# Optimization experiments

Measured on AMD Instinct MI355X. Metric: run time of the kernel, lower is better.

The kernel has to match this reference:

```python
import jax, jax.numpy as jnp
import numpy as np

NUM_HEADS = 8
DIM_OUT = 768
SCALE = DIM_OUT ** (-0.5)


def setup_inputs() -> dict:
    key = jax.random.key(0)
    k1, k2, k3, k4, k5 = jax.random.split(key, 5)
    B, N1, N2, DIM_T, DIM_V, K = 4, 2048, 2048, 768, 1024, 4
    F_t = jax.random.normal(k1, (B, N1, DIM_T), dtype=jnp.float32)
    F_s = jax.random.normal(k2, (B, N2, DIM_V), dtype=jnp.float32)
    # stacked linear_proj weights, stored input-major: x @ W_lin[layer]
    W_lin = jax.random.normal(k3, (K, DIM_V, DIM_T), dtype=jnp.float32) * 0.02
    # conv1d(kernel=1) == pointwise linear, stored input-major: x @ W_q + b_q
    W_q = jax.random.normal(k4, (DIM_T, DIM_OUT), dtype=jnp.float32) * 0.02
    b_q = jax.random.normal(k5, (DIM_OUT,), dtype=jnp.float32) * 0.02
    layer = 1
    return {"F_t": F_t, "F_s": F_s, "W_lin": W_lin, "W_q": W_q, "b_q": b_q, "layer": layer}


def reference(F_t, F_s, W_lin, W_q, b_q, layer):
    B, N1, _ = F_t.shape
    N2 = F_s.shape[1]
    H = NUM_HEADS
    D = DIM_OUT // H  # head_dim

    # per-layer linear projection + L2 normalization of keys/values
    F_s_p = F_s @ W_lin[layer]                                   # [B,N2,dim_t]
    F_s_p = F_s_p / jnp.linalg.norm(F_s_p, axis=-1, keepdims=True)

    # conv1d kernel-size-1 Q projection == pointwise linear
    q = (F_t @ W_q + b_q).reshape(B, N1, H, D)                   # [B,N1,H,D]
    kv = F_s_p.reshape(B, N2, H, D)                              # [B,N2,H,D]

    attn = jnp.einsum('bnhd,bmhd->bhnm', q, kv) * SCALE          # [B,H,N1,N2]
    attn = jax.nn.softmax(attn, axis=-1)

    F_t_a = jnp.einsum('bhnm,bmhd->bnhd', attn, kv).reshape(B, N1, H * D)
    F_t_a = F_t_a + F_t                                          # residual
    F_t_a = F_t_a / jnp.linalg.norm(F_t_a, axis=-1, keepdims=True)
    return (F_t_a, F_s_p)
```

## Files before the change

### kernel.cpp

```cpp
#include <hip/hip_runtime.h>

using short8 = __attribute__((ext_vector_type(8))) short;
using f32x4  = __attribute__((ext_vector_type(4))) float;

#define DEV __device__ __forceinline__

#define GLBP(p) ((const __attribute__((address_space(1))) unsigned int*)(p))
#define LDSP(p) ((__attribute__((address_space(3))) unsigned int*)(p))

#define EXP2F(x) __builtin_amdgcn_exp2f(x)

DEV unsigned short f2bf(float f) {
    unsigned int u = __float_as_uint(f);
    u += 0x7fffu + ((u >> 16) & 1u);
    return (unsigned short)(u >> 16);
}

DEV unsigned int pack2bf(float a, float b) {
    unsigned int ua = __float_as_uint(a);
    ua += 0x7fffu + ((ua >> 16) & 1u);
    unsigned int ub = __float_as_uint(b);
    ub += 0x7fffu + ((ub >> 16) & 1u);
    return (ua >> 16) | (ub & 0xffff0000u);
}

__global__ __launch_bounds__(256) void wt2_k(const float* __restrict__ Wl,
                                             const float* __restrict__ Wq,
                                             unsigned short* __restrict__ outl,
                                             unsigned short* __restrict__ outq,
                                             const int* __restrict__ layerp) {
    const int z = blockIdx.z;
    int R, C;
    const float* in;
    unsigned short* out;
    if (z == 0) {
        R = 1024; C = 768;
        in = Wl + (size_t)layerp[0] * (1024 * 768);
        out = outl;
    } else {
        if (blockIdx.y >= 24) return;
        R = 768; C = 768;
        in = Wq;
        out = outq;
    }
    __shared__ float t[32][33];
    const int tx = threadIdx.x & 31, ty = threadIdx.x >> 5;
    const int c0 = blockIdx.x * 32, r0 = blockIdx.y * 32;
#pragma unroll
    for (int it = 0; it < 4; ++it)
        t[ty + it * 8][tx] = in[(size_t)(r0 + ty + it * 8) * C + c0 + tx];
    __syncthreads();
#pragma unroll
    for (int it = 0; it < 4; ++it)
        out[(size_t)(c0 + ty + it * 8) * R + r0 + tx] = f2bf(t[tx][ty + it * 8]);
}

__global__ __launch_bounds__(256) void kvt_k(const unsigned short* __restrict__ kv,
                                             unsigned short* __restrict__ kvT) {
    const int n0 = blockIdx.x * 32, d0 = blockIdx.y * 32, bh = blockIdx.z;
    const int b = bh >> 3, h = bh & 7;
    __shared__ unsigned short t[32][33];
    const int tx = threadIdx.x & 31, ty = threadIdx.x >> 5;
#pragma unroll
    for (int it = 0; it < 4; ++it)
        t[ty + it * 8][tx] = kv[(size_t)(b * 2048 + n0 + ty + it * 8) * 768 + h * 96 + d0 + tx];
    __syncthreads();
#pragma unroll
    for (int it = 0; it < 4; ++it)
        kvT[((size_t)bh * 96 + d0 + ty + it * 8) * 2048 + n0 + tx] = t[tx][ty + it * 8];
}

__global__ __launch_bounds__(256) void gemm_dual(const float* __restrict__ A0,
                                                 const unsigned short* __restrict__ B0,
                                                 float* __restrict__ C0,
                                                 const float* __restrict__ A1,
                                                 const unsigned short* __restrict__ B1,
                                                 unsigned short* __restrict__ C1,
                                                 const float* __restrict__ bias,
                                                 float oscale) {
    __shared__ unsigned short smA[4096];
    __shared__ unsigned short smB[3072];
    const int z = blockIdx.z;
    const float* A = z ? A1 : A0;
    const unsigned short* B = z ? B1 : B0;
    const int K = z ? 768 : 1024;
    const int tid = threadIdx.x, lane = tid & 63;
    const int l15 = lane & 15, g = lane >> 4;
    const int w = tid >> 6, wm = w >> 1, wn = w & 1;
    const int m0 = blockIdx.x * 128, n0 = blockIdx.y * 96;
    const int srow = tid >> 2, skg = tid & 3;
    const int brow0 = tid % 96, bkg0 = tid / 96;
    const int c1 = tid + 256;
    const int brow1 = c1 % 96, bkg1 = c1 / 96;
    const unsigned short* pB0 = B + (size_t)(n0 + brow0) * K + bkg0 * 8;
    const unsigned short* pB1 = B + (size_t)(n0 + brow1) * K + bkg1 * 8;
    f32x4 acc[4][3] = {};
    const int nkt = K >> 5;
    for (int kt = 0; kt < nkt; ++kt) {
        const int k0 = kt << 5;
        __syncthreads();
        {
            __builtin_amdgcn_global_load_lds(GLBP(pB0 + k0), LDSP(smB + tid * 8), 16, 0, 0);
            if (tid < 128)
                __builtin_amdgcn_global_load_lds(GLBP(pB1 + k0), LDSP(smB + c1 * 8), 16, 0, 0);
            const float* p0 = A + (size_t)(m0 + srow) * K + k0 + skg * 8;
            const float* p1 = A + (size_t)(m0 + 64 + srow) * K + k0 + skg * 8;
            float4 a0 = *(const float4*)p0, a0b = *(const float4*)(p0 + 4);
            float4 a1 = *(const float4*)p1, a1b = *(const float4*)(p1 + 4);
            short8 va0, va1;
            va0[0] = f2bf(a0.x);  va0[1] = f2bf(a0.y);  va0[2] = f2bf(a0.z);  va0[3] = f2bf(a0.w);
            va0[4] = f2bf(a0b.x); va0[5] = f2bf(a0b.y); va0[6] = f2bf(a0b.z); va0[7] = f2bf(a0b.w);
            va1[0] = f2bf(a1.x);  va1[1] = f2bf(a1.y);  va1[2] = f2bf(a1.z);  va1[3] = f2bf(a1.w);
            va1[4] = f2bf(a1b.x); va1[5] = f2bf(a1b.y); va1[6] = f2bf(a1b.z); va1[7] = f2bf(a1b.w);
            *(short8*)(smA + (skg * 128 + srow) * 8) = va0;
            *(short8*)(smA + (skg * 128 + 64 + srow) * 8) = va1;
        }
        __syncthreads();
        short8 af[4], bf[3];
#pragma unroll
        for (int i = 0; i < 4; ++i)
            af[i] = *(const short8*)(smA + (g * 128 + wm * 64 + i * 16 + l15) * 8);
#pragma unroll
        for (int j = 0; j < 3; ++j)
            bf[j] = *(const short8*)(smB + (g * 96 + wn * 48 + j * 16 + l15) * 8);
#pragma unroll
        for (int i = 0; i < 4; ++i)
#pragma unroll
            for (int j = 0; j < 3; ++j)
                acc[i][j] = __builtin_amdgcn_mfma_f32_16x16x32_bf16(af[i], bf[j], acc[i][j], 0, 0, 0);
    }
#pragma unroll
    for (int j = 0; j < 3; ++j) {
        const int col = n0 + wn * 48 + j * 16 + l15;
        const float bv = z ? bias[col] : 0.0f;
#pragma unroll
        for (int i = 0; i < 4; ++i)
#pragma unroll
            for (int r = 0; r < 4; ++r) {
                const int row = m0 + wm * 64 + i * 16 + g * 4 + r;
                if (z == 0) {
                    C0[(size_t)row * 768 + col] = acc[i][j][r];
                } else {
                    const float v = (acc[i][j][r] + bv) * oscale;
                    C1[(size_t)row * 768 + col] = f2bf(v);
                }
            }
    }
}

__global__ __launch_bounds__(256) void rownorm_k(const float* __restrict__ in,
                                                 float* __restrict__ outf,
                                                 unsigned short* __restrict__ outb) {
    const int lane = threadIdx.x & 63;
    const int row = blockIdx.x * 4 + (threadIdx.x >> 6);
    const float* p = in + (size_t)row * 768;
    float4 v[3];
    float s = 0.f;
#pragma unroll
    for (int i = 0; i < 3; ++i) {
        v[i] = ((const float4*)p)[i * 64 + lane];
        s += v[i].x * v[i].x + v[i].y * v[i].y + v[i].z * v[i].z + v[i].w * v[i].w;
    }
#pragma unroll
    for (int mask = 1; mask < 64; mask <<= 1) s += __shfl_xor(s, mask);
    const float inv = rsqrtf(s);
    float4* of = (float4*)(outf + (size_t)row * 768);
    ushort4* ob = (ushort4*)(outb + (size_t)row * 768);
#pragma unroll
    for (int i = 0; i < 3; ++i) {
        float4 q;
        q.x = v[i].x * inv; q.y = v[i].y * inv; q.z = v[i].z * inv; q.w = v[i].w * inv;
        of[i * 64 + lane] = q;
        ushort4 u;
        u.x = f2bf(q.x); u.y = f2bf(q.y); u.z = f2bf(q.z); u.w = f2bf(q.w);
        ob[i * 64 + lane] = u;
    }
}

__global__ __launch_bounds__(256) void resid_norm_k(const unsigned short* __restrict__ in,
                                                    const float* __restrict__ res,
                                                    float* __restrict__ outf) {
    const int lane = threadIdx.x & 63;
    const int row = blockIdx.x * 4 + (threadIdx.x >> 6);
    const ushort4* pa = (const ushort4*)(in + (size_t)row * 768);
    const float4* pb = (const float4*)(res + (size_t)row * 768);
    float4 v[3];
    float s = 0.f;
#pragma unroll
    for (int i = 0; i < 3; ++i) {
        ushort4 a = pa[i * 64 + lane];
        float4 b = pb[i * 64 + lane];
        float4 c;
        c.x = __uint_as_float((unsigned int)a.x << 16) + b.x;
        c.y = __uint_as_float((unsigned int)a.y << 16) + b.y;
        c.z = __uint_as_float((unsigned int)a.z << 16) + b.z;
        c.w = __uint_as_float((unsigned int)a.w << 16) + b.w;
        v[i] = c;
        s += c.x * c.x + c.y * c.y + c.z * c.z + c.w * c.w;
    }
#pragma unroll
    for (int mask = 1; mask < 64; mask <<= 1) s += __shfl_xor(s, mask);
    const float inv = rsqrtf(s);
    float4* of = (float4*)(outf + (size_t)row * 768);
#pragma unroll
    for (int i = 0; i < 3; ++i) {
        float4 q;
        q.x = v[i].x * inv; q.y = v[i].y * inv; q.z = v[i].z * inv; q.w = v[i].w * inv;
        of[i * 64 + lane] = q;
    }
}

__global__ __launch_bounds__(512) void attn_k(const unsigned short* __restrict__ Q,
                                              const unsigned short* __restrict__ KV,
                                              const unsigned short* __restrict__ KVT,
                                              unsigned short* __restrict__ O) {
    __shared__ unsigned short sK[2][6144];
    __shared__ unsigned short sV[2][6144];
    __shared__ unsigned short plds[8][32][72];
    const int hw = blockIdx.x;
    const int bid = (hw & 7) * 32 + (hw >> 3);
    const int qb = bid & 7, h = (bid >> 3) & 7, b = bid >> 6;
    const int tid = threadIdx.x, lane = tid & 63, w = tid >> 6;
    const int l15 = lane & 15, g = lane >> 4;
    const int q0 = qb * 256 + w * 32;
    unsigned short(*pw)[72] = plds[w];

    const unsigned short* kb = KV + (size_t)(b * 2048) * 768 + h * 96;
    const unsigned short* vb = KVT + (size_t)((b * 8 + h) * 96) * 2048;

    const short8 kOnes = {(short)0x3F80, (short)0x3F80, (short)0x3F80, (short)0x3F80,
                          (short)0x3F80, (short)0x3F80, (short)0x3F80, (short)0x3F80};

    short8 aq[2][3];
#pragma unroll
    for (int mi = 0; mi < 2; ++mi) {
        const unsigned short* qp = Q + (size_t)(b * 2048 + q0 + mi * 16 + l15) * 768 + h * 96 + g * 8;
#pragma unroll
        for (int ks = 0; ks < 3; ++ks) aq[mi][ks] = *(const short8*)(qp + ks * 32);
    }
    f32x4 o[2][6] = {};
    f32x4 o6[2] = {};

    const unsigned short* sgp[3];
    int sstep[3], soff[3], sisk[3];
#pragma unroll
    for (int p = 0; p < 3; ++p) {
        const int li = p * 8 + w;
        if (li < 12) {
            sgp[p] = kb + (size_t)lane * 768 + li * 8;
            sstep[p] = 64 * 768;
            soff[p] = li * 512;
            sisk[p] = 1;
        } else {
            const int j = li - 12;
            const int i = j * 64 + lane;
            const int kvsub = i / 96, d = i - kvsub * 96;
            sgp[p] = vb + (size_t)d * 2048 + kvsub * 8;
            sstep[p] = 64;
            soff[p] = j * 512;
            sisk[p] = 0;
        }
    }
    auto stage = [&](unsigned short* sKb, unsigned short* sVb) {
#pragma unroll
        for (int p = 0; p < 3; ++p) {
            __builtin_amdgcn_global_load_lds(GLBP(sgp[p]), LDSP((sisk[p] ? sKb : sVb) + soff[p]), 16, 0, 0);
            sgp[p] += sstep[p];
        }
    };

    stage(sK[0], sV[0]);
    __syncthreads();

    for (int c = 0; c < 32; ++c) {
        const int cur = c & 1;
        const unsigned short* sKb = sK[cur];
        const unsigned short* sVb = sV[cur];
        if (c < 31) stage(sK[cur ^ 1], sV[cur ^ 1]);

        f32x4 s[2][4];
        __builtin_amdgcn_s_setprio(1);
#pragma unroll
        for (int t = 0; t < 4; ++t) {
            short8 k0 = *(const short8*)(sKb + ((0 + g) * 64 + t * 16 + l15) * 8);
            short8 k1 = *(const short8*)(sKb + ((4 + g) * 64 + t * 16 + l15) * 8);
            short8 k2 = *(const short8*)(sKb + ((8 + g) * 64 + t * 16 + l15) * 8);
#pragma unroll
            for (int mi = 0; mi < 2; ++mi) {
                f32x4 a = {};
                a = __builtin_amdgcn_mfma_f32_16x16x32_bf16(k0, aq[mi][0], a, 0, 0, 0);
                a = __builtin_amdgcn_mfma_f32_16x16x32_bf16(k1, aq[mi][1], a, 0, 0, 0);
                a = __builtin_amdgcn_mfma_f32_16x16x32_bf16(k2, aq[mi][2], a, 0, 0, 0);
                s[mi][t] = a;
            }
        }
        __builtin_amdgcn_s_setprio(0);
#pragma unroll
        for (int mi = 0; mi < 2; ++mi) {
#pragma unroll
            for (int t = 0; t < 4; ++t)
#pragma unroll
                for (int r = 0; r < 4; ++r)
                    s[mi][t][r] = EXP2F(s[mi][t][r]);
#pragma unroll
            for (int t = 0; t < 4; ++t) {
                uint2 pk;
                pk.x = pack2bf(s[mi][t][0], s[mi][t][1]);
                pk.y = pack2bf(s[mi][t][2], s[mi][t][3]);
                *(uint2*)&pw[mi * 16 + l15][t * 16 + g * 4] = pk;
            }
        }
        __builtin_amdgcn_s_setprio(1);
#pragma unroll
        for (int half = 0; half < 2; ++half) {
            short8 pa[2];
#pragma unroll
            for (int mi = 0; mi < 2; ++mi) {
                pa[mi] = *(const short8*)&pw[mi * 16 + l15][half * 32 + g * 8];
                o6[mi] = __builtin_amdgcn_mfma_f32_16x16x32_bf16(pa[mi], kOnes, o6[mi], 0, 0, 0);
            }
#pragma unroll
            for (int dt = 0; dt < 6; ++dt) {
                short8 bv = *(const short8*)(sVb + ((half * 4 + g) * 96 + dt * 16 + l15) * 8);
#pragma unroll
                for (int mi = 0; mi < 2; ++mi)
                    o[mi][dt] = __builtin_amdgcn_mfma_f32_16x16x32_bf16(pa[mi], bv, o[mi][dt], 0, 0, 0);
            }
        }
        __builtin_amdgcn_s_setprio(0);
        __syncthreads();
    }
#pragma unroll
    for (int mi = 0; mi < 2; ++mi)
#pragma unroll
        for (int r = 0; r < 4; ++r) {
            const float inv = 1.0f / o6[mi][r];
            unsigned short* op = O + (size_t)(b * 2048 + q0 + mi * 16 + g * 4 + r) * 768 + h * 96 + l15;
#pragma unroll
            for (int dt = 0; dt < 6; ++dt) op[dt * 16] = f2bf(o[mi][dt][r] * inv);
        }
}

#define SCALE_F 0.05205877254075156f

extern "C" void kernel_launch(void* const* d_in, const int* in_sizes, int n_in,
                              void* d_out, int out_size, void* d_ws, size_t ws_size,
                              hipStream_t stream) {
    const float* Ft = (const float*)d_in[0];
    const float* Fs = (const float*)d_in[1];
    const float* Wl = (const float*)d_in[2];
    const float* Wq = (const float*)d_in[3];
    const float* bq = (const float*)d_in[4];
    const int* layer = (const int*)d_in[5];

    float* out0 = (float*)d_out;
    float* out1 = out0 + 6291456;

    char* ws = (char*)d_ws;
    unsigned short* wsQ   = (unsigned short*)(ws);
    unsigned short* wsWlt = (unsigned short*)(ws + 12582912);
    unsigned short* wsWqt = (unsigned short*)(ws + 14155776);
    unsigned short* wsKV  = (unsigned short*)(ws + 15335424);
    unsigned short* wsKVT = (unsigned short*)(ws + 27918336);
    float*          wsTmp = (float*)(ws + 40501248);
    unsigned short* wsOb  = (unsigned short*)wsTmp;

    wt2_k<<<dim3(24, 32, 2), 256, 0, stream>>>(Wl, Wq, wsWlt, wsWqt, layer);
    gemm_dual<<<dim3(64, 8, 2), 256, 0, stream>>>(Fs, wsWlt, wsTmp, Ft, wsWqt, wsQ, bq, SCALE_F);
    rownorm_k<<<2048, 256, 0, stream>>>(wsTmp, out1, wsKV);
    kvt_k<<<dim3(64, 3, 32), 256, 0, stream>>>(wsKV, wsKVT);
    attn_k<<<256, 512, 0, stream>>>(wsQ, wsKV, wsKVT, wsOb);
    resid_norm_k<<<2048, 256, 0, stream>>>(wsOb, Ft, out0);
}
```

Measured before the change: 145.3 us.

## Pre-convert activations to bf16 and double-buffer GEMM with async LDS loads

Adds a separate conversion kernel that turns F_s and F_t into bf16 in workspace, so the dual GEMM can load A tiles with global_load_lds directly instead of converting fp32 in registers. The GEMM now double-buffers A and B in shared memory, issuing the next stage's loads before computing the current one, and raises wave priority around the MFMA block. The fp32 projection output is written straight into the output buffer and normalised in place, which drops the temporary buffer. The trade is an extra kernel launch and an extra read and write of both activation tensors, plus double the LDS footprint.

```diff
diff --git a/kernel.cpp b/kernel.cpp
--- a/kernel.cpp
+++ b/kernel.cpp
@@ -22,6 +22,23 @@
     unsigned int ub = __float_as_uint(b);
     ub += 0x7fffu + ((ub >> 16) & 1u);
     return (ua >> 16) | (ub & 0xffff0000u);
+}
+
+__global__ __launch_bounds__(256) void cvt2_k(const float* __restrict__ in0,
+                                              unsigned short* __restrict__ out0, int n40,
+                                              const float* __restrict__ in1,
+                                              unsigned short* __restrict__ out1, int n41) {
+    const float* in = blockIdx.z ? in1 : in0;
+    unsigned short* out = blockIdx.z ? out1 : out0;
+    const int n4 = blockIdx.z ? n41 : n40;
+    int i = blockIdx.x * blockDim.x + threadIdx.x;
+    const int stride = gridDim.x * blockDim.x;
+    for (; i < n4; i += stride) {
+        float4 v = ((const float4*)in)[i];
+        ushort4 o;
+        o.x = f2bf(v.x); o.y = f2bf(v.y); o.z = f2bf(v.z); o.w = f2bf(v.w);
+        ((ushort4*)out)[i] = o;
+    }
 }
 
 __global__ __launch_bounds__(256) void wt2_k(const float* __restrict__ Wl,
@@ -70,64 +87,61 @@
         kvT[((size_t)bh * 96 + d0 + ty + it * 8) * 2048 + n0 + tx] = t[tx][ty + it * 8];
 }
 
-__global__ __launch_bounds__(256) void gemm_dual(const float* __restrict__ A0,
+__global__ __launch_bounds__(256) void gemm_dual(const unsigned short* __restrict__ A0,
                                                  const unsigned short* __restrict__ B0,
                                                  float* __restrict__ C0,
-                                                 const float* __restrict__ A1,
+                                                 const unsigned short* __restrict__ A1,
                                                  const unsigned short* __restrict__ B1,
                                                  unsigned short* __restrict__ C1,
                                                  const float* __restrict__ bias,
                                                  float oscale) {
-    __shared__ unsigned short smA[4096];
-    __shared__ unsigned short smB[3072];
+    __shared__ unsigned short smA[2][4096];
+    __shared__ unsigned short smB[2][3072];
     const int z = blockIdx.z;
-    const float* A = z ? A1 : A0;
+    const unsigned short* A = z ? A1 : A0;
     const unsigned short* B = z ? B1 : B0;
     const int K = z ? 768 : 1024;
+    const int nkt = K >> 5;
     const int tid = threadIdx.x, lane = tid & 63;
     const int l15 = lane & 15, g = lane >> 4;
     const int w = tid >> 6, wm = w >> 1, wn = w & 1;
     const int m0 = blockIdx.x * 128, n0 = blockIdx.y * 96;
-    const int srow = tid >> 2, skg = tid & 3;
-    const int brow0 = tid % 96, bkg0 = tid / 96;
+    const unsigned short* pA0 = A + (size_t)(m0 + (w & 1) * 64 + lane) * K + (w >> 1) * 8;
+    const unsigned short* pA1 = pA0 + 16;
+    const int oa0 = w * 512;
+    const int oa1 = w * 512 + 2048;
     const int c1 = tid + 256;
-    const int brow1 = c1 % 96, bkg1 = c1 / 96;
-    const unsigned short* pB0 = B + (size_t)(n0 + brow0) * K + bkg0 * 8;
-    const unsigned short* pB1 = B + (size_t)(n0 + brow1) * K + bkg1 * 8;
+    const unsigned short* pB0 = B + (size_t)(n0 + tid % 96) * K + (tid / 96) * 8;
+    const unsigned short* pB1 = B + (size_t)(n0 + c1 % 96) * K + (c1 / 96) * 8;
     f32x4 acc[4][3] = {};
-    const int nkt = K >> 5;
+    auto stage = [&](int buf) {
+        __builtin_amdgcn_global_load_lds(GLBP(pA0), LDSP(smA[buf] + oa0), 16, 0, 0);
+        __builtin_amdgcn_global_load_lds(GLBP(pA1), LDSP(smA[buf] + oa1), 16, 0, 0);
+        __builtin_amdgcn_global_load_lds(GLBP(pB0), LDSP(smB[buf] + tid * 8), 16, 0, 0);
+        if (tid < 128)
+            __builtin_amdgcn_global_load_lds(GLBP(pB1), LDSP(smB[buf] + c1 * 8), 16, 0, 0);
+        pA0 += 32; pA1 += 32; pB0 += 32; pB1 += 32;
+    };
+    stage(0);
+    __syncthreads();
     for (int kt = 0; kt < nkt; ++kt) {
-        const int k0 = kt << 5;
-        __syncthreads();
-        {
-            __builtin_amdgcn_global_load_lds(GLBP(pB0 + k0), LDSP(smB + tid * 8), 16, 0, 0);
-            if (tid < 128)
-                __builtin_amdgcn_global_load_lds(GLBP(pB1 + k0), LDSP(smB + c1 * 8), 16, 0, 0);
-            const float* p0 = A + (size_t)(m0 + srow) * K + k0 + skg * 8;
-            const float* p1 = A + (size_t)(m0 + 64 + srow) * K + k0 + skg * 8;
-            float4 a0 = *(const float4*)p0, a0b = *(const float4*)(p0 + 4);
-            float4 a1 = *(const float4*)p1, a1b = *(const float4*)(p1 + 4);
-            short8 va0, va1;
-            va0[0] = f2bf(a0.x);  va0[1] = f2bf(a0.y);  va0[2] = f2bf(a0.z);  va0[3] = f2bf(a0.w);
-            va0[4] = f2bf(a0b.x); va0[5] = f2bf(a0b.y); va0[6] = f2bf(a0b.z); va0[7] = f2bf(a0b.w);
-            va1[0] = f2bf(a1.x);  va1[1] = f2bf(a1.y);  va1[2] = f2bf(a1.z);  va1[3] = f2bf(a1.w);
-            va1[4] = f2bf(a1b.x); va1[5] = f2bf(a1b.y); va1[6] = f2bf(a1b.z); va1[7] = f2bf(a1b.w);
-            *(short8*)(smA + (skg * 128 + srow) * 8) = va0;
-            *(short8*)(smA + (skg * 128 + 64 + srow) * 8) = va1;
-        }
-        __syncthreads();
+        const int cur = kt & 1;
+        if (kt + 1 < nkt) stage(cur ^ 1);
         short8 af[4], bf[3];
 #pragma unroll
         for (int i = 0; i < 4; ++i)
-            af[i] = *(const short8*)(smA + (g * 128 + wm * 64 + i * 16 + l15) * 8);
+            af[i] = *(const short8*)(smA[cur] + (g * 128 + wm * 64 + i * 16 + l15) * 8);
 #pragma unroll
         for (int j = 0; j < 3; ++j)
-            bf[j] = *(const short8*)(smB + (g * 96 + wn * 48 + j * 16 + l15) * 8);
+            bf[j] = *(const short8*)(smB[cur] + (g * 96 + wn * 48 + j * 16 + l15) * 8);
+        __builtin_amdgcn_s_setprio(1);
 #pragma unroll
         for (int i = 0; i < 4; ++i)
 #pragma unroll
             for (int j = 0; j < 3; ++j)
                 acc[i][j] = __builtin_amdgcn_mfma_f32_16x16x32_bf16(af[i], bf[j], acc[i][j], 0, 0, 0);
+        __builtin_amdgcn_s_setprio(0);
+        __syncthreads();
     }
 #pragma unroll
     for (int j = 0; j < 3; ++j) {
@@ -357,17 +371,19 @@
     float* out1 = out0 + 6291456;
 
     char* ws = (char*)d_ws;
-    unsigned short* wsQ   = (unsigned short*)(ws);
-    unsigned short* wsWlt = (unsigned short*)(ws + 12582912);
-    unsigned short* wsWqt = (unsigned short*)(ws + 14155776);
-    unsigned short* wsKV  = (unsigned short*)(ws + 15335424);
-    unsigned short* wsKVT = (unsigned short*)(ws + 27918336);
-    float*          wsTmp = (float*)(ws + 40501248);
-    unsigned short* wsOb  = (unsigned short*)wsTmp;
+    unsigned short* wsFs  = (unsigned short*)(ws);
+    unsigned short* wsFt  = (unsigned short*)(ws + 16777216);
+    unsigned short* wsQ   = (unsigned short*)(ws + 29360128);
+    unsigned short* wsWlt = (unsigned short*)(ws + 41943040);
+    unsigned short* wsWqt = (unsigned short*)(ws + 43515904);
+    unsigned short* wsKV  = (unsigned short*)(ws + 44695552);
+    unsigned short* wsKVT = (unsigned short*)(ws + 57278464);
+    unsigned short* wsOb  = wsFs;
 
     wt2_k<<<dim3(24, 32, 2), 256, 0, stream>>>(Wl, Wq, wsWlt, wsWqt, layer);
-    gemm_dual<<<dim3(64, 8, 2), 256, 0, stream>>>(Fs, wsWlt, wsTmp, Ft, wsWqt, wsQ, bq, SCALE_F);
-    rownorm_k<<<2048, 256, 0, stream>>>(wsTmp, out1, wsKV);
+    cvt2_k<<<dim3(2048, 1, 2), 256, 0, stream>>>(Fs, wsFs, 8388608 / 4, Ft, wsFt, 6291456 / 4);
+    gemm_dual<<<dim3(64, 8, 2), 256, 0, stream>>>(wsFs, wsWlt, out1, wsFt, wsWqt, wsQ, bq, SCALE_F);
+    rownorm_k<<<2048, 256, 0, stream>>>(out1, out1, wsKV);
     kvt_k<<<dim3(64, 3, 32), 256, 0, stream>>>(wsKV, wsKVT);
     attn_k<<<256, 512, 0, stream>>>(wsQ, wsKV, wsKVT, wsOb);
     resid_norm_k<<<2048, 256, 0, stream>>>(wsOb, Ft, out0);
```

Measured after the change: 166.3 us. +14.4%, slower.

## Double-buffer gemm_dual LDS tiles with register prefetch and write projection in place

Applied to the files above, without the earlier changes.

The projection GEMM now uses two LDS buffers and stages the next K-tile through registers, writing tile k+1 while computing on tile k. This drops one barrier per iteration and overlaps global loads with MFMA work. B-tile loading moves from direct global-to-LDS loads to register loads, and MFMA sections get raised wave priority. The F_s projection is also written straight into the output buffer and normalized in place, removing a scratch buffer. The cost is more registers, which could lower occupancy, and rownorm_k now reads and writes the same buffer.

```diff
diff --git a/kernel.cpp b/kernel.cpp
--- a/kernel.cpp
+++ b/kernel.cpp
@@ -78,56 +78,72 @@
                                                  unsigned short* __restrict__ C1,
                                                  const float* __restrict__ bias,
                                                  float oscale) {
-    __shared__ unsigned short smA[4096];
-    __shared__ unsigned short smB[3072];
+    __shared__ unsigned short smA[2][4096];
+    __shared__ unsigned short smB[2][3072];
     const int z = blockIdx.z;
     const float* A = z ? A1 : A0;
     const unsigned short* B = z ? B1 : B0;
     const int K = z ? 768 : 1024;
+    const int nkt = K >> 5;
     const int tid = threadIdx.x, lane = tid & 63;
     const int l15 = lane & 15, g = lane >> 4;
     const int w = tid >> 6, wm = w >> 1, wn = w & 1;
     const int m0 = blockIdx.x * 128, n0 = blockIdx.y * 96;
-    const int srow = tid >> 2, skg = tid & 3;
-    const int brow0 = tid % 96, bkg0 = tid / 96;
+    const float* pA0 = A + (size_t)(m0 + (w & 1) * 64 + lane) * K + (w >> 1) * 8;
+    const float* pA1 = pA0 + 16;
+    const int oa0 = (w * 64 + lane) * 8;
+    const int oa1 = oa0 + 2048;
     const int c1 = tid + 256;
-    const int brow1 = c1 % 96, bkg1 = c1 / 96;
-    const unsigned short* pB0 = B + (size_t)(n0 + brow0) * K + bkg0 * 8;
-    const unsigned short* pB1 = B + (size_t)(n0 + brow1) * K + bkg1 * 8;
+    const unsigned short* pB0 = B + (size_t)(n0 + tid % 96) * K + (tid / 96) * 8;
+    const unsigned short* pB1 = B + (size_t)(n0 + c1 % 96) * K + (c1 / 96) * 8;
+    const bool hb1 = (tid < 128);
+
+    float4 ra0, ra1, ra2, ra3;
+    short8 rb0, rb1;
+    auto loadT = [&]() {
+        ra0 = *(const float4*)pA0; ra1 = *(const float4*)(pA0 + 4);
+        ra2 = *(const float4*)pA1; ra3 = *(const float4*)(pA1 + 4);
+        rb0 = *(const short8*)pB0;
+        if (hb1) rb1 = *(const short8*)pB1;
+        pA0 += 32; pA1 += 32; pB0 += 32; pB1 += 32;
+    };
+    auto writeT = [&](int buf) {
+        short8 va0, va1;
+        va0[0] = f2bf(ra0.x); va0[1] = f2bf(ra0.y); va0[2] = f2bf(ra0.z); va0[3] = f2bf(ra0.w);
+        va0[4] = f2bf(ra1.x); va0[5] = f2bf(ra1.y); va0[6] = f2bf(ra1.z); va0[7] = f2bf(ra1.w);
+        va1[0] = f2bf(ra2.x); va1[1] = f2bf(ra2.y); va1[2] = f2bf(ra2.z); va1[3] = f2bf(ra2.w);
+        va1[4] = f2bf(ra3.x); va1[5] = f2bf(ra3.y); va1[6] = f2bf(ra3.z); va1[7] = f2bf(ra3.w);
+        *(short8*)(smA[buf] + oa0) = va0;
+        *(short8*)(smA[buf] + oa1) = va1;
+        *(short8*)(smB[buf] + tid * 8) = rb0;
+        if (hb1) *(short8*)(smB[buf] + c1 * 8) = rb1;
+    };
+
+    loadT();
+    writeT(0);
+    loadT();
+    __syncthreads();
+
     f32x4 acc[4][3] = {};
-    const int nkt = K >> 5;
     for (int kt = 0; kt < nkt; ++kt) {
-        const int k0 = kt << 5;
-        __syncthreads();
-        {
-            __builtin_amdgcn_global_load_lds(GLBP(pB0 + k0), LDSP(smB + tid * 8), 16, 0, 0);
-            if (tid < 128)
-                __builtin_amdgcn_global_load_lds(GLBP(pB1 + k0), LDSP(smB + c1 * 8), 16, 0, 0);
-            const float* p0 = A + (size_t)(m0 + srow) * K + k0 + skg * 8;
-            const float* p1 = A + (size_t)(m0 + 64 + srow) * K + k0 + skg * 8;
-            float4 a0 = *(const float4*)p0, a0b = *(const float4*)(p0 + 4);
-            float4 a1 = *(const float4*)p1, a1b = *(const float4*)(p1 + 4);
-            short8 va0, va1;
-            va0[0] = f2bf(a0.x);  va0[1] = f2bf(a0.y);  va0[2] = f2bf(a0.z);  va0[3] = f2bf(a0.w);
-            va0[4] = f2bf(a0b.x); va0[5] = f2bf(a0b.y); va0[6] = f2bf(a0b.z); va0[7] = f2bf(a0b.w);
-            va1[0] = f2bf(a1.x);  va1[1] = f2bf(a1.y);  va1[2] = f2bf(a1.z);  va1[3] = f2bf(a1.w);
-            va1[4] = f2bf(a1b.x); va1[5] = f2bf(a1b.y); va1[6] = f2bf(a1b.z); va1[7] = f2bf(a1b.w);
-            *(short8*)(smA + (skg * 128 + srow) * 8) = va0;
-            *(short8*)(smA + (skg * 128 + 64 + srow) * 8) = va1;
-        }
-        __syncthreads();
+        const int cur = kt & 1;
+        if (kt + 1 < nkt) writeT(cur ^ 1);
+        if (kt + 2 < nkt) loadT();
         short8 af[4], bf[3];
 #pragma unroll
         for (int i = 0; i < 4; ++i)
-            af[i] = *(const short8*)(smA + (g * 128 + wm * 64 + i * 16 + l15) * 8);
+            af[i] = *(const short8*)(smA[cur] + (g * 128 + wm * 64 + i * 16 + l15) * 8);
 #pragma unroll
         for (int j = 0; j < 3; ++j)
-            bf[j] = *(const short8*)(smB + (g * 96 + wn * 48 + j * 16 + l15) * 8);
+            bf[j] = *(const short8*)(smB[cur] + (g * 96 + wn * 48 + j * 16 + l15) * 8);
+        __builtin_amdgcn_s_setprio(1);
 #pragma unroll
         for (int i = 0; i < 4; ++i)
 #pragma unroll
             for (int j = 0; j < 3; ++j)
                 acc[i][j] = __builtin_amdgcn_mfma_f32_16x16x32_bf16(af[i], bf[j], acc[i][j], 0, 0, 0);
+        __builtin_amdgcn_s_setprio(0);
+        __syncthreads();
     }
 #pragma unroll
     for (int j = 0; j < 3; ++j) {
@@ -362,12 +378,11 @@
     unsigned short* wsWqt = (unsigned short*)(ws + 14155776);
     unsigned short* wsKV  = (unsigned short*)(ws + 15335424);
     unsigned short* wsKVT = (unsigned short*)(ws + 27918336);
-    float*          wsTmp = (float*)(ws + 40501248);
-    unsigned short* wsOb  = (unsigned short*)wsTmp;
+    unsigned short* wsOb  = (unsigned short*)(ws + 40501248);
 
     wt2_k<<<dim3(24, 32, 2), 256, 0, stream>>>(Wl, Wq, wsWlt, wsWqt, layer);
-    gemm_dual<<<dim3(64, 8, 2), 256, 0, stream>>>(Fs, wsWlt, wsTmp, Ft, wsWqt, wsQ, bq, SCALE_F);
-    rownorm_k<<<2048, 256, 0, stream>>>(wsTmp, out1, wsKV);
+    gemm_dual<<<dim3(64, 8, 2), 256, 0, stream>>>(Fs, wsWlt, out1, Ft, wsWqt, wsQ, bq, SCALE_F);
+    rownorm_k<<<2048, 256, 0, stream>>>(out1, out1, wsKV);
     kvt_k<<<dim3(64, 3, 32), 256, 0, stream>>>(wsKV, wsKVT);
     attn_k<<<256, 512, 0, stream>>>(wsQ, wsKV, wsKVT, wsOb);
     resid_norm_k<<<2048, 256, 0, stream>>>(wsOb, Ft, out0);
```

After: 183.6 us. +26.3%, slower.
